# Optimization experiments

Measured on AMD Instinct MI355X. Metric: run time of the kernel, lower is better.

Reference implementation:

```python
import jax, jax.numpy as jnp
import numpy as np

B, N, DIM, NL, E = 8, 4096, 128, 3, 524288
NN = B * N


def setup_inputs() -> dict:
    key = jax.random.key(0)
    kx, ke, kw = jax.random.split(key, 3)
    x = jax.random.normal(kx, (B, N, DIM), dtype=jnp.float32)
    batch_edge_index = jax.random.randint(ke, (2, E), 0, NN, dtype=jnp.int32)
    wks = jax.random.split(kw, NL)
    Ws = jnp.stack([jax.random.normal(k, (DIM, DIM), dtype=jnp.float32) / np.sqrt(DIM)
                    for k in wks])  # [NL, DIM, DIM]
    bs = jnp.zeros((NL, DIM), dtype=jnp.float32)
    return {"x": x, "batch_edge_index": batch_edge_index, "Ws": Ws, "bs": bs}


def _gcn_layer(x, W, b, row, col, deg_inv_sqrt, n):
    # PyG GCNConv: h = x @ W; symmetric normalization over edges+self-loops;
    # scatter-add messages at targets (col); add bias.
    h = x @ W  # [n, DIM]
    norm = deg_inv_sqrt[row] * deg_inv_sqrt[col]  # [E+n]
    msg = h[row] * norm[:, None]  # gather at sources, scale
    return jax.ops.segment_sum(msg, col, num_segments=n) + b


def reference(x, batch_edge_index, Ws, bs):
    nb, npts, d = x.shape
    n = nb * npts
    h = x.reshape(n, d)
    # add self-loops once (same edge structure for all layers)
    loops = jnp.arange(n, dtype=batch_edge_index.dtype)
    row = jnp.concatenate([batch_edge_index[0], loops])
    col = jnp.concatenate([batch_edge_index[1], loops])
    deg = jax.ops.segment_sum(jnp.ones_like(col, dtype=h.dtype), col, num_segments=n)
    deg_inv_sqrt = jnp.where(deg > 0, jax.lax.rsqrt(jnp.maximum(deg, 1e-12)), 0.0)
    for i in range(NL):
        out = _gcn_layer(h, Ws[i], bs[i], row, col, deg_inv_sqrt, n)
        h = jax.nn.relu(h + out)  # residual + relu (dropout = identity in eval)
    return h.reshape(nb, npts, d)
```

## Files before the change

kernel.cpp:

```cpp
#include <hip/hip_runtime.h>


typedef __attribute__((ext_vector_type(8))) short short8;
typedef __attribute__((ext_vector_type(4))) float f32x4;
typedef __attribute__((ext_vector_type(2))) float f32x2;

__device__ inline ushort f2bf(float f) {
    union { float f; unsigned u; } v; v.f = f;
    unsigned u = v.u;
    return (ushort)((u + 0x7fffu + ((u >> 16) & 1u)) >> 16);
}
__device__ inline float2 bf2f(unsigned u) {
    union { unsigned i; float f; } a, b;
    a.i = u << 16;
    b.i = u & 0xffff0000u;
    return make_float2(a.f, b.f);
}
__device__ inline f32x4 bf4(uint2 v) {
    float2 a = bf2f(v.x), b = bf2f(v.y);
    f32x4 r = { a.x, a.y, b.x, b.y };
    return r;
}
__device__ inline short8 pack8(f32x4 a, f32x4 b) {
    short8 r = { (short)f2bf(a.x), (short)f2bf(a.y), (short)f2bf(a.z), (short)f2bf(a.w),
                 (short)f2bf(b.x), (short)f2bf(b.y), (short)f2bf(b.z), (short)f2bf(b.w) };
    return r;
}
__device__ inline unsigned char f2fp8(float f) {
    return (unsigned char)(__builtin_amdgcn_cvt_pk_fp8_f32(f, f, 0, false) & 0xff);
}
__device__ inline f32x4 fp8x4(unsigned v) {
    f32x2 lo = __builtin_amdgcn_cvt_pk_f32_fp8((int)v, false);
    f32x2 hi = __builtin_amdgcn_cvt_pk_f32_fp8((int)v, true);
    f32x4 r = { lo.x, lo.y, hi.x, hi.y };
    return r;
}

__global__ void k_deg(const int* __restrict__ col, int* __restrict__ deg, int E) {
    int i = blockIdx.x * blockDim.x + threadIdx.x;
    if (i < E) atomicAdd(&deg[col[i]], 1);
}

__global__ __launch_bounds__(256) void k_scan1(const int* __restrict__ deg,
                                               int* __restrict__ offs,
                                               int* __restrict__ bsum, int n) {
    __shared__ int sm[256];
    int t = threadIdx.x, i = blockIdx.x * 256 + t;
    int v = (i < n) ? deg[i] : 0;
    sm[t] = v;
    __syncthreads();
    for (int off = 1; off < 256; off <<= 1) {
        int u = (t >= off) ? sm[t - off] : 0;
        __syncthreads();
        sm[t] += u;
        __syncthreads();
    }
    if (i < n) offs[i] = sm[t] - v;
    if (t == 255) bsum[blockIdx.x] = sm[255];
}

__global__ __launch_bounds__(128) void k_scan2(int* __restrict__ bsum, int nb) {
    __shared__ int sm[128];
    int t = threadIdx.x;
    int v = (t < nb) ? bsum[t] : 0;
    sm[t] = v;
    __syncthreads();
    for (int off = 1; off < 128; off <<= 1) {
        int u = (t >= off) ? sm[t - off] : 0;
        __syncthreads();
        sm[t] += u;
        __syncthreads();
    }
    if (t < nb) bsum[t] = sm[t] - v;
}

__global__ __launch_bounds__(256) void k_scan3(int* __restrict__ offs,
                                               const int* __restrict__ bsum,
                                               const int* __restrict__ deg,
                                               int* __restrict__ cnt,
                                               float* __restrict__ dis,
                                               unsigned* __restrict__ g32,
                                               int n, int E) {
    int i = blockIdx.x * 256 + threadIdx.x;
    if (i < n) {
        int o = offs[i] + bsum[blockIdx.x];
        offs[i] = o;
        cnt[i] = o;
        dis[i] = rsqrtf((float)(deg[i] + 1));
    }
    if (i == 0) offs[n] = E;
    if (i < 32) g32[(size_t)n * 32 + i] = 0;
}

__global__ void k_csr(const int* __restrict__ row, const int* __restrict__ col,
                      int* __restrict__ cnt, ushort* __restrict__ csru, int E) {
    int i = blockIdx.x * blockDim.x + threadIdx.x;
    if (i < E) {
        int c = col[i];
        int p = atomicAdd(&cnt[c], 1);
        csru[p] = (ushort)row[i];
    }
}

#define GEMM_BODY(A0, A1, A2, A3)                                               \
    f32x4 acc[8] = {};                                                          \
    _Pragma("unroll")                                                           \
    for (int nf = 0; nf < 8; ++nf) {                                            \
        const unsigned* wr = &Wl[nf * 16 + c][0];                               \
        int sx = (c & 7) << 2;                                                  \
        int b = q * 4;                                                          \
        short8 b0 = *(const short8*)(wr + ((b +  0) ^ sx));                     \
        short8 b1 = *(const short8*)(wr + ((b + 16) ^ sx));                     \
        short8 b2 = *(const short8*)(wr + ((b + 32) ^ sx));                     \
        short8 b3 = *(const short8*)(wr + ((b + 48) ^ sx));                     \
        acc[nf] = __builtin_amdgcn_mfma_f32_16x16x32_bf16(A0, b0, acc[nf], 0, 0, 0); \
        acc[nf] = __builtin_amdgcn_mfma_f32_16x16x32_bf16(A1, b1, acc[nf], 0, 0, 0); \
        acc[nf] = __builtin_amdgcn_mfma_f32_16x16x32_bf16(A2, b2, acc[nf], 0, 0, 0); \
        acc[nf] = __builtin_amdgcn_mfma_f32_16x16x32_bf16(A3, b3, acc[nf], 0, 0, 0); \
    }                                                                           \
    float d0 = dis[rb + q * 4 + 0], d1 = dis[rb + q * 4 + 1];                   \
    float d2 = dis[rb + q * 4 + 2], d3 = dis[rb + q * 4 + 3];                   \
    _Pragma("unroll")                                                           \
    for (int nf = 0; nf < 8; ++nf) {                                            \
        int gc = nf * 16 + c;                                                   \
        g[(size_t)(rb + q * 4 + 0) * 128 + gc] = f2fp8(acc[nf][0] * d0);        \
        g[(size_t)(rb + q * 4 + 1) * 128 + gc] = f2fp8(acc[nf][1] * d1);        \
        g[(size_t)(rb + q * 4 + 2) * 128 + gc] = f2fp8(acc[nf][2] * d2);        \
        g[(size_t)(rb + q * 4 + 3) * 128 + gc] = f2fp8(acc[nf][3] * d3);        \
    }

#define W_STAGE                                                                  \
    __shared__ unsigned Wl[128][64];                                             \
    int tid = threadIdx.x;                                                       \
    {                                                                            \
        int nn = tid & 127, hf = tid >> 7;                                       \
        for (int qq = 0; qq < 32; ++qq) {                                        \
            int k2 = hf * 32 + qq;                                               \
            float lo = W[(size_t)(2 * k2) * 128 + nn];                           \
            float hi = W[(size_t)(2 * k2 + 1) * 128 + nn];                       \
            Wl[nn][k2 ^ ((nn & 7) << 2)] = ((unsigned)f2bf(hi) << 16) | f2bf(lo);\
        }                                                                        \
    }                                                                            \
    __syncthreads();                                                             \
    int w = tid >> 6, l = tid & 63;                                              \
    int rb = blockIdx.x * 64 + w * 16;                                           \
    int c = l & 15, q = l >> 4;

__global__ __launch_bounds__(256) void k_gemm(const unsigned* __restrict__ hb,
                                              const float* __restrict__ W,
                                              const float* __restrict__ dis,
                                              unsigned char* __restrict__ g, int n) {
    W_STAGE
    const short8* arow = (const short8*)(hb + (size_t)(rb + c) * 64);
    short8 a0 = arow[q], a1 = arow[4 + q], a2 = arow[8 + q], a3 = arow[12 + q];
    GEMM_BODY(a0, a1, a2, a3)
}

__global__ __launch_bounds__(256) void k_gemm0(const float* __restrict__ x,
                                               const float* __restrict__ W,
                                               const float* __restrict__ dis,
                                               unsigned char* __restrict__ g, int n) {
    W_STAGE
    const f32x4* xr = (const f32x4*)(x + (size_t)(rb + c) * 128);
    short8 a0 = pack8(xr[q * 2 +  0], xr[q * 2 +  1]);
    short8 a1 = pack8(xr[q * 2 +  8], xr[q * 2 +  9]);
    short8 a2 = pack8(xr[q * 2 + 16], xr[q * 2 + 17]);
    short8 a3 = pack8(xr[q * 2 + 24], xr[q * 2 + 25]);
    GEMM_BODY(a0, a1, a2, a3)
}

__global__ __launch_bounds__(256) void k_gather(const unsigned* __restrict__ g,
                                                unsigned* __restrict__ hb,
                                                const float* __restrict__ dis,
                                                const float* __restrict__ bias,
                                                const int* __restrict__ offs,
                                                const ushort* __restrict__ csru,
                                                const float* __restrict__ xres,
                                                float* __restrict__ outp,
                                                int n, int use_x, int last) {
    int wid = threadIdx.x >> 6, lane = threadIdx.x & 63;
    int node = blockIdx.x * 4 + wid;
    if (node >= n) return;
    int half = lane >> 5, fl = lane & 31;
    int fo4 = fl * 4;
    const char* gb = (const char*)g;

    unsigned sv = *(const unsigned*)(gb + ((size_t)(half ? n : node) << 7) + fo4);
    f32x4 acc = fp8x4(sv);

    int s = offs[node];
    int deg = offs[node + 1] - s;
    for (int j0 = 0; j0 < deg; j0 += 64) {
        int rem = deg - j0;
        int m = rem < 64 ? rem : 64;
        int idx = (lane < m) ? (int)__builtin_nontemporal_load(&csru[s + j0 + lane]) : n;
        int mc = (m + 15) & ~15;
        for (int t = 0; t < mc; t += 16) {
            unsigned v[8];
#pragma unroll
            for (int u = 0; u < 8; ++u) {
                int r = __shfl(idx, t + 2 * u + half, 64);
                v[u] = *(const unsigned*)(gb + ((size_t)r << 7) + fo4);
            }
            f32x4 s0 = (fp8x4(v[0]) + fp8x4(v[1])) + (fp8x4(v[2]) + fp8x4(v[3]));
            f32x4 s1 = (fp8x4(v[4]) + fp8x4(v[5])) + (fp8x4(v[6]) + fp8x4(v[7]));
            acc += s0 + s1;
        }
    }
    acc.x += __shfl_xor(acc.x, 32, 64);
    acc.y += __shfl_xor(acc.y, 32, 64);
    acc.z += __shfl_xor(acc.z, 32, 64);
    acc.w += __shfl_xor(acc.w, 32, 64);

    if (half == 0) {
        float d = dis[node];
        f32x4 bv = ((const f32x4*)bias)[fl];
        f32x4 hv;
        if (use_x) {
            hv = ((const f32x4*)xres)[(size_t)node * 32 + fl];
        } else {
            uint2 h2 = *(const uint2*)((const char*)hb + ((size_t)node << 8) + fl * 8);
            hv = bf4(h2);
        }
        f32x4 o = acc * d + hv + bv;
        o.x = fmaxf(o.x, 0.f); o.y = fmaxf(o.y, 0.f);
        o.z = fmaxf(o.z, 0.f); o.w = fmaxf(o.w, 0.f);
        if (last) {
            __builtin_nontemporal_store(o, (f32x4*)&outp[(size_t)node * 128 + fl * 4]);
        } else {
            uint2 pk;
            pk.x = ((unsigned)f2bf(o.y) << 16) | f2bf(o.x);
            pk.y = ((unsigned)f2bf(o.w) << 16) | f2bf(o.z);
            *(uint2*)((char*)hb + ((size_t)node << 8) + fl * 8) = pk;
        }
    }
}

static inline size_t al256(size_t x) { return (x + 255) & ~(size_t)255; }

extern "C" void kernel_launch(void* const* d_in, const int* in_sizes, int n_in,
                              void* d_out, int out_size, void* d_ws, size_t ws_size,
                              hipStream_t stream) {
    const float* x  = (const float*)d_in[0];
    const int*   ei = (const int*)d_in[1];
    const float* Ws = (const float*)d_in[2];
    const float* bs = (const float*)d_in[3];
    int n  = in_sizes[0] / 128;
    int E  = in_sizes[1] / 2;
    int NL = in_sizes[2] / (128 * 128);
    const int* rowp = ei;
    const int* colp = ei + E;

    char* ws = (char*)d_ws;
    size_t gplane  = al256((size_t)(n + 1) * 128);
    size_t hplane  = al256((size_t)(n + 1) * 256);
    unsigned* g  = (unsigned*)ws;
    unsigned* hb = (unsigned*)(ws + gplane);
    char* p = ws + gplane + hplane;
    float* dis  = (float*)p;               p += al256((size_t)n * 4);
    int*   deg  = (int*)p;                 p += al256((size_t)n * 4);
    int*   offs = (int*)p;                 p += al256((size_t)(n + 1) * 4);
    int*   cnt  = (int*)p;                 p += al256((size_t)n * 4);
    int*   bsum = (int*)p;                 p += 512;
    ushort* csru = (ushort*)p;

    int nb = (n + 255) / 256;

    (void)hipMemsetAsync(deg, 0, (size_t)n * 4, stream);
    k_deg<<<(E + 255) / 256, 256, 0, stream>>>(colp, deg, E);
    k_scan1<<<nb, 256, 0, stream>>>(deg, offs, bsum, n);
    k_scan2<<<1, 128, 0, stream>>>(bsum, nb);
    k_scan3<<<nb, 256, 0, stream>>>(offs, bsum, deg, cnt, dis, g, n, E);
    k_csr<<<(E + 255) / 256, 256, 0, stream>>>(rowp, colp, cnt, csru, E);

    for (int l = 0; l < NL; ++l) {
        int last = (l + 1 == NL);
        const float* Wl = Ws + (size_t)l * 128 * 128;
        if (l == 0)
            k_gemm0<<<n / 64, 256, 0, stream>>>(x, Wl, dis, (unsigned char*)g, n);
        else
            k_gemm<<<n / 64, 256, 0, stream>>>(hb, Wl, dis, (unsigned char*)g, n);
        k_gather<<<(n + 3) / 4, 256, 0, stream>>>(g, hb, dis,
                                                  bs + (size_t)l * 128,
                                                  offs, csru, x,
                                                  (float*)d_out, n,
                                                  l == 0, last);
    }
}
```

Measured before the change: 151.2 us.

## Fuse degree count into layer-0 GEMM, fold scan2, move source norm into gather

Layer 0's GEMM no longer needs dis, so it is merged with the degree-count atomics into one launch, with extra blocks doing the atomics. The separate block-sum scan kernel is removed: each scan3 block reduces the preceding block sums itself. The GEMM now stores unscaled fp8 values, and the gather applies each source node's normalization per edge through a shuffled dis lookup. The gather is restructured so each lane owns two features and all 64 lanes walk every edge, which drops the half-wave split and the final cross-half reduction. The trade-off is an extra dis load and an FMA per edge, plus narrower 2-byte gather loads.

New measurement: 150.3 us. Within noise of the previous version (-0.6%).

```diff
diff --git a/kernel.cpp b/kernel.cpp
--- a/kernel.cpp
+++ b/kernel.cpp
@@ -16,11 +16,6 @@
     b.i = u & 0xffff0000u;
     return make_float2(a.f, b.f);
 }
-__device__ inline f32x4 bf4(uint2 v) {
-    float2 a = bf2f(v.x), b = bf2f(v.y);
-    f32x4 r = { a.x, a.y, b.x, b.y };
-    return r;
-}
 __device__ inline short8 pack8(f32x4 a, f32x4 b) {
     short8 r = { (short)f2bf(a.x), (short)f2bf(a.y), (short)f2bf(a.z), (short)f2bf(a.w),
                  (short)f2bf(b.x), (short)f2bf(b.y), (short)f2bf(b.z), (short)f2bf(b.w) };
@@ -29,16 +24,9 @@
 __device__ inline unsigned char f2fp8(float f) {
     return (unsigned char)(__builtin_amdgcn_cvt_pk_fp8_f32(f, f, 0, false) & 0xff);
 }
-__device__ inline f32x4 fp8x4(unsigned v) {
+__device__ inline float2 fp8x2(ushort v) {
     f32x2 lo = __builtin_amdgcn_cvt_pk_f32_fp8((int)v, false);
-    f32x2 hi = __builtin_amdgcn_cvt_pk_f32_fp8((int)v, true);
-    f32x4 r = { lo.x, lo.y, hi.x, hi.y };
-    return r;
-}
-
-__global__ void k_deg(const int* __restrict__ col, int* __restrict__ deg, int E) {
-    int i = blockIdx.x * blockDim.x + threadIdx.x;
-    if (i < E) atomicAdd(&deg[col[i]], 1);
+    return make_float2(lo.x, lo.y);
 }
 
 __global__ __launch_bounds__(256) void k_scan1(const int* __restrict__ deg,
@@ -59,21 +47,6 @@
     if (t == 255) bsum[blockIdx.x] = sm[255];
 }
 
-__global__ __launch_bounds__(128) void k_scan2(int* __restrict__ bsum, int nb) {
-    __shared__ int sm[128];
-    int t = threadIdx.x;
-    int v = (t < nb) ? bsum[t] : 0;
-    sm[t] = v;
-    __syncthreads();
-    for (int off = 1; off < 128; off <<= 1) {
-        int u = (t >= off) ? sm[t - off] : 0;
-        __syncthreads();
-        sm[t] += u;
-        __syncthreads();
-    }
-    if (t < nb) bsum[t] = sm[t] - v;
-}
-
 __global__ __launch_bounds__(256) void k_scan3(int* __restrict__ offs,
                                                const int* __restrict__ bsum,
                                                const int* __restrict__ deg,
@@ -81,9 +54,18 @@
                                                float* __restrict__ dis,
                                                unsigned* __restrict__ g32,
                                                int n, int E) {
-    int i = blockIdx.x * 256 + threadIdx.x;
+    __shared__ int red[256];
+    int t = threadIdx.x, bid = blockIdx.x;
+    red[t] = (t < 128 && t < bid) ? bsum[t] : 0;
+    __syncthreads();
+    for (int off = 128; off >= 1; off >>= 1) {
+        if (t < off) red[t] += red[t + off];
+        __syncthreads();
+    }
+    int base = red[0];
+    int i = bid * 256 + t;
     if (i < n) {
-        int o = offs[i] + bsum[blockIdx.x];
+        int o = offs[i] + base;
         offs[i] = o;
         cnt[i] = o;
         dis[i] = rsqrtf((float)(deg[i] + 1));
@@ -118,18 +100,16 @@
         acc[nf] = __builtin_amdgcn_mfma_f32_16x16x32_bf16(A2, b2, acc[nf], 0, 0, 0); \
         acc[nf] = __builtin_amdgcn_mfma_f32_16x16x32_bf16(A3, b3, acc[nf], 0, 0, 0); \
     }                                                                           \
-    float d0 = dis[rb + q * 4 + 0], d1 = dis[rb + q * 4 + 1];                   \
-    float d2 = dis[rb + q * 4 + 2], d3 = dis[rb + q * 4 + 3];                   \
     _Pragma("unroll")                                                           \
     for (int nf = 0; nf < 8; ++nf) {                                            \
         int gc = nf * 16 + c;                                                   \
-        g[(size_t)(rb + q * 4 + 0) * 128 + gc] = f2fp8(acc[nf][0] * d0);        \
-        g[(size_t)(rb + q * 4 + 1) * 128 + gc] = f2fp8(acc[nf][1] * d1);        \
-        g[(size_t)(rb + q * 4 + 2) * 128 + gc] = f2fp8(acc[nf][2] * d2);        \
-        g[(size_t)(rb + q * 4 + 3) * 128 + gc] = f2fp8(acc[nf][3] * d3);        \
-    }
-
-#define W_STAGE                                                                  \
+        g[(size_t)(rb + q * 4 + 0) * 128 + gc] = f2fp8(acc[nf][0]);             \
+        g[(size_t)(rb + q * 4 + 1) * 128 + gc] = f2fp8(acc[nf][1]);             \
+        g[(size_t)(rb + q * 4 + 2) * 128 + gc] = f2fp8(acc[nf][2]);             \
+        g[(size_t)(rb + q * 4 + 3) * 128 + gc] = f2fp8(acc[nf][3]);             \
+    }
+
+#define W_STAGE(TILE)                                                            \
     __shared__ unsigned Wl[128][64];                                             \
     int tid = threadIdx.x;                                                       \
     {                                                                            \
@@ -143,24 +123,31 @@
     }                                                                            \
     __syncthreads();                                                             \
     int w = tid >> 6, l = tid & 63;                                              \
-    int rb = blockIdx.x * 64 + w * 16;                                           \
+    int rb = (TILE) * 64 + w * 16;                                               \
     int c = l & 15, q = l >> 4;
 
 __global__ __launch_bounds__(256) void k_gemm(const unsigned* __restrict__ hb,
                                               const float* __restrict__ W,
-                                              const float* __restrict__ dis,
                                               unsigned char* __restrict__ g, int n) {
-    W_STAGE
+    W_STAGE(blockIdx.x)
     const short8* arow = (const short8*)(hb + (size_t)(rb + c) * 64);
     short8 a0 = arow[q], a1 = arow[4 + q], a2 = arow[8 + q], a3 = arow[12 + q];
     GEMM_BODY(a0, a1, a2, a3)
 }
 
-__global__ __launch_bounds__(256) void k_gemm0(const float* __restrict__ x,
-                                               const float* __restrict__ W,
-                                               const float* __restrict__ dis,
-                                               unsigned char* __restrict__ g, int n) {
-    W_STAGE
+__global__ __launch_bounds__(256) void k_l0(const float* __restrict__ x,
+                                            const float* __restrict__ W,
+                                            unsigned char* __restrict__ g,
+                                            const int* __restrict__ col,
+                                            int* __restrict__ deg,
+                                            int n, int E) {
+    int gtiles = n >> 6;
+    if ((int)blockIdx.x >= gtiles) {
+        int i = ((int)blockIdx.x - gtiles) * 256 + threadIdx.x;
+        if (i < E) atomicAdd(&deg[col[i]], 1);
+        return;
+    }
+    W_STAGE((int)blockIdx.x)
     const f32x4* xr = (const f32x4*)(x + (size_t)(rb + c) * 128);
     short8 a0 = pack8(xr[q * 2 +  0], xr[q * 2 +  1]);
     short8 a1 = pack8(xr[q * 2 +  8], xr[q * 2 +  9]);
@@ -169,7 +156,7 @@
     GEMM_BODY(a0, a1, a2, a3)
 }
 
-__global__ __launch_bounds__(256) void k_gather(const unsigned* __restrict__ g,
+__global__ __launch_bounds__(256) void k_gather(const ushort* __restrict__ g,
                                                 unsigned* __restrict__ hb,
                                                 const float* __restrict__ dis,
                                                 const float* __restrict__ bias,
@@ -181,58 +168,57 @@
     int wid = threadIdx.x >> 6, lane = threadIdx.x & 63;
     int node = blockIdx.x * 4 + wid;
     if (node >= n) return;
-    int half = lane >> 5, fl = lane & 31;
-    int fo4 = fl * 4;
-    const char* gb = (const char*)g;
-
-    unsigned sv = *(const unsigned*)(gb + ((size_t)(half ? n : node) << 7) + fo4);
-    f32x4 acc = fp8x4(sv);
-
+
+    float dn = dis[node];
+    float2 acc;
+    {
+        float2 f = fp8x2(g[(size_t)node * 64 + lane]);
+        acc.x = f.x * dn; acc.y = f.y * dn;
+    }
     int s = offs[node];
     int deg = offs[node + 1] - s;
     for (int j0 = 0; j0 < deg; j0 += 64) {
         int rem = deg - j0;
         int m = rem < 64 ? rem : 64;
-        int idx = (lane < m) ? (int)__builtin_nontemporal_load(&csru[s + j0 + lane]) : n;
+        int idx = n; float dsl = 0.f;
+        if (lane < m) {
+            idx = (int)__builtin_nontemporal_load(&csru[s + j0 + lane]);
+            dsl = dis[idx];
+        }
         int mc = (m + 15) & ~15;
         for (int t = 0; t < mc; t += 16) {
-            unsigned v[8];
+            ushort v[16];
 #pragma unroll
-            for (int u = 0; u < 8; ++u) {
-                int r = __shfl(idx, t + 2 * u + half, 64);
-                v[u] = *(const unsigned*)(gb + ((size_t)r << 7) + fo4);
+            for (int u = 0; u < 16; ++u) {
+                int r = __shfl(idx, t + u, 64);
+                v[u] = g[(size_t)r * 64 + lane];
             }
-            f32x4 s0 = (fp8x4(v[0]) + fp8x4(v[1])) + (fp8x4(v[2]) + fp8x4(v[3]));
-            f32x4 s1 = (fp8x4(v[4]) + fp8x4(v[5])) + (fp8x4(v[6]) + fp8x4(v[7]));
-            acc += s0 + s1;
+            float ds[16];
+#pragma unroll
+            for (int u = 0; u < 16; ++u) ds[u] = __shfl(dsl, t + u, 64);
+#pragma unroll
+            for (int u = 0; u < 16; ++u) {
+                float2 f = fp8x2(v[u]);
+                acc.x = fmaf(f.x, ds[u], acc.x);
+                acc.y = fmaf(f.y, ds[u], acc.y);
+            }
         }
     }
-    acc.x += __shfl_xor(acc.x, 32, 64);
-    acc.y += __shfl_xor(acc.y, 32, 64);
-    acc.z += __shfl_xor(acc.z, 32, 64);
-    acc.w += __shfl_xor(acc.w, 32, 64);
-
-    if (half == 0) {
-        float d = dis[node];
-        f32x4 bv = ((const f32x4*)bias)[fl];
-        f32x4 hv;
-        if (use_x) {
-            hv = ((const f32x4*)xres)[(size_t)node * 32 + fl];
-        } else {
-            uint2 h2 = *(const uint2*)((const char*)hb + ((size_t)node << 8) + fl * 8);
-            hv = bf4(h2);
-        }
-        f32x4 o = acc * d + hv + bv;
-        o.x = fmaxf(o.x, 0.f); o.y = fmaxf(o.y, 0.f);
-        o.z = fmaxf(o.z, 0.f); o.w = fmaxf(o.w, 0.f);
-        if (last) {
-            __builtin_nontemporal_store(o, (f32x4*)&outp[(size_t)node * 128 + fl * 4]);
-        } else {
-            uint2 pk;
-            pk.x = ((unsigned)f2bf(o.y) << 16) | f2bf(o.x);
-            pk.y = ((unsigned)f2bf(o.w) << 16) | f2bf(o.z);
-            *(uint2*)((char*)hb + ((size_t)node << 8) + fl * 8) = pk;
-        }
+
+    float2 bv = ((const float2*)bias)[lane];
+    float2 hv;
+    if (use_x) {
+        hv = ((const float2*)xres)[(size_t)node * 64 + lane];
+    } else {
+        hv = bf2f(hb[(size_t)node * 64 + lane]);
+    }
+    float ox = fmaxf(hv.x + acc.x * dn + bv.x, 0.f);
+    float oy = fmaxf(hv.y + acc.y * dn + bv.y, 0.f);
+    if (last) {
+        f32x2 o = { ox, oy };
+        __builtin_nontemporal_store(o, (f32x2*)&outp[(size_t)node * 128 + lane * 2]);
+    } else {
+        hb[(size_t)node * 64 + lane] = ((unsigned)f2bf(oy) << 16) | f2bf(ox);
     }
 }
 
@@ -254,8 +240,8 @@
     char* ws = (char*)d_ws;
     size_t gplane  = al256((size_t)(n + 1) * 128);
     size_t hplane  = al256((size_t)(n + 1) * 256);
-    unsigned* g  = (unsigned*)ws;
-    unsigned* hb = (unsigned*)(ws + gplane);
+    unsigned char* g  = (unsigned char*)ws;
+    unsigned*      hb = (unsigned*)(ws + gplane);
     char* p = ws + gplane + hplane;
     float* dis  = (float*)p;               p += al256((size_t)n * 4);
     int*   deg  = (int*)p;                 p += al256((size_t)n * 4);
@@ -265,22 +251,21 @@
     ushort* csru = (ushort*)p;
 
     int nb = (n + 255) / 256;
+    int gtiles = n / 64;
+    int eblocks = (E + 255) / 256;
 
     (void)hipMemsetAsync(deg, 0, (size_t)n * 4, stream);
-    k_deg<<<(E + 255) / 256, 256, 0, stream>>>(colp, deg, E);
+    k_l0<<<gtiles + eblocks, 256, 0, stream>>>(x, Ws, g, colp, deg, n, E);
     k_scan1<<<nb, 256, 0, stream>>>(deg, offs, bsum, n);
-    k_scan2<<<1, 128, 0, stream>>>(bsum, nb);
-    k_scan3<<<nb, 256, 0, stream>>>(offs, bsum, deg, cnt, dis, g, n, E);
-    k_csr<<<(E + 255) / 256, 256, 0, stream>>>(rowp, colp, cnt, csru, E);
+    k_scan3<<<nb, 256, 0, stream>>>(offs, bsum, deg, cnt, dis, (unsigned*)g, n, E);
+    k_csr<<<eblocks, 256, 0, stream>>>(rowp, colp, cnt, csru, E);
 
     for (int l = 0; l < NL; ++l) {
         int last = (l + 1 == NL);
-        const float* Wl = Ws + (size_t)l * 128 * 128;
-        if (l == 0)
-            k_gemm0<<<n / 64, 256, 0, stream>>>(x, Wl, dis, (unsigned char*)g, n);
-        else
-            k_gemm<<<n / 64, 256, 0, stream>>>(hb, Wl, dis, (unsigned char*)g, n);
-        k_gather<<<(n + 3) / 4, 256, 0, stream>>>(g, hb, dis,
+        if (l > 0)
+            k_gemm<<<gtiles, 256, 0, stream>>>(hb, Ws + (size_t)l * 128 * 128,
+                                               g, n);
+        k_gather<<<(n + 3) / 4, 256, 0, stream>>>((const ushort*)g, hb, dis,
                                                   bs + (size_t)l * 128,
                                                   offs, csru, x,
                                                   (float*)d_out, n,
```
